# Optimization experiments

Measured on AMD Instinct MI355X. Metric: run time of the kernel, lower is better.

The kernel has to match this reference:

```python
import jax, jax.numpy as jnp
import numpy as np
import math

B, H, L, D = 4, 16, 8192, 64


def setup_inputs() -> dict:
    key = jax.random.key(0)
    kq, kk, kv, kmu = jax.random.split(key, 4)
    Q = jax.random.normal(kq, (B, H, L, D), dtype=jnp.float32)
    K = jax.random.normal(kk, (B, H, L, D), dtype=jnp.float32)
    V = jax.random.normal(kv, (B, H, L, D), dtype=jnp.float32)
    mask = jnp.ones((B, L), dtype=jnp.float32)
    # learned params (multi_gauss=True): pi init [0.5,0.5]; mu ~ N(0,0.5) with mu[0]=0
    pi = jnp.array([0.5, 0.5], dtype=jnp.float32)
    mu = jax.random.normal(kmu, (2, H, D), dtype=jnp.float32) * 0.5
    mu = mu * jnp.array([0.0, 1.0], dtype=jnp.float32)[:, None, None]
    return {"Q": Q, "K": K, "V": V, "mask": mask, "pi": pi, "mu": mu}


def reference(Q, K, V, mask, pi, mu):
    # mixture-of-Gaussian keys: shift K by two learned means, convex-combine
    p = jnp.clip(pi, 0.0, 1.0)
    K1 = K - mu[0][None, :, None, :]
    K2 = K - mu[1][None, :, None, :]
    Km = K1 * p[0] + K2 * p[1]
    # kernelized linear attention: phi(x) = elu(x)+1, scaled by 1/L^0.25
    L_ = Q.shape[2]
    s = 1.0 / math.sqrt(math.sqrt(L_))
    m = mask[:, None, :, None]  # [B,1,L,1]
    Qf = (jax.nn.elu(Q) + 1.0) * s
    Kf = (jax.nn.elu(Km) + 1.0) * m * s
    Vm = V * m
    # K^T V first: [B,H,D,D] state, then Q @ state -> [B,H,L,D]
    KV = jnp.einsum('bhld,bhle->bhde', Kf, Vm)
    return jnp.einsum('bhld,bhde->bhle', Qf, KV)
```

## Files before the change

kernel.cpp:

```cpp
#include <hip/hip_runtime.h>
#include <cstddef>

#define B_ 4
#define H_ 16
#define L_ 8192
#define D_ 64
#define BH_ (B_ * H_)

#define SCALE 0.1051120519067143f

__device__ __forceinline__ float elu1(float x) {
    return x > 0.0f ? (x + 1.0f) : __expf(x);
}

__global__ __launch_bounds__(256) void zero_kernel(float4* __restrict__ p) {
    p[(size_t)blockIdx.x * 256 + threadIdx.x] = make_float4(0.f, 0.f, 0.f, 0.f);
}

__global__ __launch_bounds__(256) void kv_kernel(
    const float* __restrict__ K, const float* __restrict__ V,
    const float* __restrict__ mask, const float* __restrict__ pi,
    const float* __restrict__ mu, float* __restrict__ kv)
{
    const int bh = blockIdx.x;
    const int b = bh >> 4;
    const int h = bh & 15;
    const int l0 = blockIdx.y * 512;
    const int t = threadIdx.x;
    const int lane_e = t & 63;
    const int dbase = (t >> 6) * 16;

    __shared__ float muc[64];
    __shared__ float sK[32][64];
    __shared__ float sV[32][64];

    float p0 = fminf(fmaxf(pi[0], 0.f), 1.f);
    float p1 = fminf(fmaxf(pi[1], 0.f), 1.f);
    const float psum = p0 + p1;
    if (t < 64) {
        muc[t] = p0 * mu[h * D_ + t] + p1 * mu[(H_ + h) * D_ + t];
    }
    __syncthreads();

    const float* Kb = K + (size_t)bh * L_ * D_;
    const float* Vb = V + (size_t)bh * L_ * D_;
    const float* mb = mask + (size_t)b * L_;

    const int r0 = t >> 4;
    const int c0 = (t & 15) * 4;
    const int r1 = (t + 256) >> 4;
    const int c1 = c0;

    const float4 mu0 = *(const float4*)&muc[c0];
    const float4 mu1 = *(const float4*)&muc[c1];

    float acc[16];
#pragma unroll
    for (int i = 0; i < 16; ++i) acc[i] = 0.f;

    for (int tile = 0; tile < 512; tile += 32) {
        const int lb = l0 + tile;
        {
            const int l = lb + r0;
            const float m = mb[l];
            const float sm = SCALE * m;
            float4 k = *(const float4*)(Kb + (size_t)l * D_ + c0);
            float4 o;
            o.x = elu1(k.x * psum - mu0.x) * sm;
            o.y = elu1(k.y * psum - mu0.y) * sm;
            o.z = elu1(k.z * psum - mu0.z) * sm;
            o.w = elu1(k.w * psum - mu0.w) * sm;
            *(float4*)&sK[r0][c0] = o;
            float4 v = *(const float4*)(Vb + (size_t)l * D_ + c0);
            v.x *= m; v.y *= m; v.z *= m; v.w *= m;
            *(float4*)&sV[r0][c0] = v;
        }
        {
            const int l = lb + r1;
            const float m = mb[l];
            const float sm = SCALE * m;
            float4 k = *(const float4*)(Kb + (size_t)l * D_ + c1);
            float4 o;
            o.x = elu1(k.x * psum - mu1.x) * sm;
            o.y = elu1(k.y * psum - mu1.y) * sm;
            o.z = elu1(k.z * psum - mu1.z) * sm;
            o.w = elu1(k.w * psum - mu1.w) * sm;
            *(float4*)&sK[r1][c1] = o;
            float4 v = *(const float4*)(Vb + (size_t)l * D_ + c1);
            v.x *= m; v.y *= m; v.z *= m; v.w *= m;
            *(float4*)&sV[r1][c1] = v;
        }
        __syncthreads();

#pragma unroll
        for (int l = 0; l < 32; ++l) {
            const float v = sV[l][lane_e];
            const float4 ka = *(const float4*)&sK[l][dbase];
            const float4 kb = *(const float4*)&sK[l][dbase + 4];
            const float4 kc = *(const float4*)&sK[l][dbase + 8];
            const float4 kd = *(const float4*)&sK[l][dbase + 12];
            acc[0]  += ka.x * v;  acc[1]  += ka.y * v;
            acc[2]  += ka.z * v;  acc[3]  += ka.w * v;
            acc[4]  += kb.x * v;  acc[5]  += kb.y * v;
            acc[6]  += kb.z * v;  acc[7]  += kb.w * v;
            acc[8]  += kc.x * v;  acc[9]  += kc.y * v;
            acc[10] += kc.z * v;  acc[11] += kc.w * v;
            acc[12] += kd.x * v;  acc[13] += kd.y * v;
            acc[14] += kd.z * v;  acc[15] += kd.w * v;
        }
        __syncthreads();
    }

    float* kvp = kv + (size_t)bh * (D_ * D_);
#pragma unroll
    for (int j = 0; j < 16; ++j)
        atomicAdd(kvp + (dbase + j) * D_ + lane_e, acc[j]);
}

__global__ __launch_bounds__(256) void out_kernel(
    const float* __restrict__ Q, const float* __restrict__ kv,
    float* __restrict__ out)
{
    const int bh = blockIdx.x;
    const int l0 = blockIdx.y * 64;
    const int t = threadIdx.x;

    __shared__ float sKV[64][64];
    __shared__ float sQ[64][65];

    const float* Qb = Q + (size_t)bh * L_ * D_ + (size_t)l0 * D_;
    const float* kvp = kv + (size_t)bh * (D_ * D_);

#pragma unroll
    for (int i = 0; i < 4; ++i) {
        const int idx = t + i * 256;
        *(float4*)&sKV[idx >> 4][(idx & 15) * 4] = *(const float4*)(kvp + (size_t)idx * 4);
    }
#pragma unroll
    for (int i = 0; i < 4; ++i) {
        const int idx = t + i * 256;
        const int row = idx >> 4;
        const int col = (idx & 15) * 4;
        const float4 q = *(const float4*)(Qb + (size_t)idx * 4);
        sQ[row][col + 0] = elu1(q.x) * SCALE;
        sQ[row][col + 1] = elu1(q.y) * SCALE;
        sQ[row][col + 2] = elu1(q.z) * SCALE;
        sQ[row][col + 3] = elu1(q.w) * SCALE;
    }
    __syncthreads();

    const int te = t & 15;
    const int tl = t >> 4;
    const int e0 = te * 4;
    const int lb = tl * 4;

    float acc[16];
#pragma unroll
    for (int i = 0; i < 16; ++i) acc[i] = 0.f;

#pragma unroll 16
    for (int d = 0; d < 64; ++d) {
        const float4 k4 = *(const float4*)&sKV[d][e0];
        const float q0 = sQ[lb + 0][d];
        const float q1 = sQ[lb + 1][d];
        const float q2 = sQ[lb + 2][d];
        const float q3 = sQ[lb + 3][d];
        acc[0]  += q0 * k4.x;  acc[1]  += q0 * k4.y;
        acc[2]  += q0 * k4.z;  acc[3]  += q0 * k4.w;
        acc[4]  += q1 * k4.x;  acc[5]  += q1 * k4.y;
        acc[6]  += q1 * k4.z;  acc[7]  += q1 * k4.w;
        acc[8]  += q2 * k4.x;  acc[9]  += q2 * k4.y;
        acc[10] += q2 * k4.z;  acc[11] += q2 * k4.w;
        acc[12] += q3 * k4.x;  acc[13] += q3 * k4.y;
        acc[14] += q3 * k4.z;  acc[15] += q3 * k4.w;
    }

    float* ob = out + (size_t)bh * L_ * D_ + (size_t)l0 * D_;
#pragma unroll
    for (int i = 0; i < 4; ++i) {
        float4 r;
        r.x = acc[i * 4 + 0];
        r.y = acc[i * 4 + 1];
        r.z = acc[i * 4 + 2];
        r.w = acc[i * 4 + 3];
        *(float4*)(ob + (size_t)(lb + i) * D_ + e0) = r;
    }
}

extern "C" void kernel_launch(void* const* d_in, const int* in_sizes, int n_in,
                              void* d_out, int out_size, void* d_ws, size_t ws_size,
                              hipStream_t stream) {
    (void)in_sizes; (void)n_in; (void)out_size; (void)ws_size;
    const float* Q    = (const float*)d_in[0];
    const float* K    = (const float*)d_in[1];
    const float* V    = (const float*)d_in[2];
    const float* mask = (const float*)d_in[3];
    const float* pi   = (const float*)d_in[4];
    const float* mu   = (const float*)d_in[5];
    float* out = (float*)d_out;
    float* kvw = (float*)d_ws;

    zero_kernel<<<256, 256, 0, stream>>>((float4*)kvw);
    kv_kernel<<<dim3(BH_, 16), 256, 0, stream>>>(K, V, mask, pi, mu, kvw);
    out_kernel<<<dim3(BH_, 128), 256, 0, stream>>>(Q, kvw, out);
}
```

Baseline: 436.7 us.

## Use 8x8 register tiles in both kernels and bf16 LDS staging for output

The KV-state kernel now gives each thread an 8x8 register tile of the DxD outer product. V is read straight from global memory and only transformed K is staged in LDS. Per-wave partial states are reduced in shared memory before one atomic pass per block. The output kernel handles 256 rows per block with an 8x8 tile per thread, storing Q (transposed) and the KV state as bf16 in LDS to halve LDS traffic. The goal is fewer LDS reads per FMA and less atomic contention, at the cost of bf16 rounding error in the output and high register pressure from 64 accumulators.

```diff
diff --git a/kernel.cpp b/kernel.cpp
--- a/kernel.cpp
+++ b/kernel.cpp
@@ -1,189 +1,209 @@
 #include <hip/hip_runtime.h>
 #include <cstddef>
+#include <stdint.h>
 
 #define B_ 4
 #define H_ 16
 #define L_ 8192
 #define D_ 64
-#define BH_ (B_ * H_)
+#define BH_ 64
 
 #define SCALE 0.1051120519067143f
 
 __device__ __forceinline__ float elu1(float x) {
     return x > 0.0f ? (x + 1.0f) : __expf(x);
 }
+__device__ __forceinline__ unsigned short f2bf_rne(float x) {
+    unsigned u = __float_as_uint(x);
+    u += 0x7fffu + ((u >> 16) & 1u);
+    return (unsigned short)(u >> 16);
+}
+__device__ __forceinline__ float bf_lo(unsigned w) { return __uint_as_float(w << 16); }
+__device__ __forceinline__ float bf_hi(unsigned w) { return __uint_as_float(w & 0xffff0000u); }
 
 __global__ __launch_bounds__(256) void zero_kernel(float4* __restrict__ p) {
     p[(size_t)blockIdx.x * 256 + threadIdx.x] = make_float4(0.f, 0.f, 0.f, 0.f);
 }
 
-__global__ __launch_bounds__(256) void kv_kernel(
+#define CH1 16
+#define ROWS1 (L_ / CH1)
+#define TR1 64
+#define SKLD 68
+
+__global__ __launch_bounds__(256, 4) void kv_kernel(
     const float* __restrict__ K, const float* __restrict__ V,
     const float* __restrict__ mask, const float* __restrict__ pi,
     const float* __restrict__ mu, float* __restrict__ kv)
 {
+    __shared__ float sK[TR1 * SKLD];
+    __shared__ float muc[64];
+
     const int bh = blockIdx.x;
-    const int b = bh >> 4;
-    const int h = bh & 15;
-    const int l0 = blockIdx.y * 512;
-    const int t = threadIdx.x;
-    const int lane_e = t & 63;
-    const int dbase = (t >> 6) * 16;
-
-    __shared__ float muc[64];
-    __shared__ float sK[32][64];
-    __shared__ float sV[32][64];
-
-    float p0 = fminf(fmaxf(pi[0], 0.f), 1.f);
-    float p1 = fminf(fmaxf(pi[1], 0.f), 1.f);
+    const int b  = bh >> 4;
+    const int h  = bh & 15;
+    const int l0 = blockIdx.y * ROWS1;
+    const int t  = threadIdx.x;
+    const int wave = t >> 6;
+    const int lane = t & 63;
+    const int d0 = (lane >> 3) * 8;
+    const int e0 = (lane & 7) * 8;
+
+    const float p0 = fminf(fmaxf(pi[0], 0.f), 1.f);
+    const float p1 = fminf(fmaxf(pi[1], 0.f), 1.f);
     const float psum = p0 + p1;
-    if (t < 64) {
-        muc[t] = p0 * mu[h * D_ + t] + p1 * mu[(H_ + h) * D_ + t];
-    }
+    if (t < 64) muc[t] = p0 * mu[h * 64 + t] + p1 * mu[1024 + h * 64 + t];
+
+    const float* Kb = K + (size_t)bh * (L_ * 64);
+    const float* Vb = V + (size_t)bh * (L_ * 64);
+    const float* mb = mask + (size_t)b * L_;
+
+    const int trow = t >> 2;
+    const int tc   = (t & 3) * 16;
+
+    float acc[64];
+#pragma unroll
+    for (int i = 0; i < 64; ++i) acc[i] = 0.f;
+
+#pragma unroll 1
+    for (int tile = 0; tile < ROWS1; tile += TR1) {
+        const int base = l0 + tile;
+        __syncthreads();
+        {
+            const int row = base + trow;
+            const float m = mb[row];
+            const float sm2 = SCALE * m * m;
+            const float* kp = Kb + (size_t)row * 64 + tc;
+#pragma unroll
+            for (int q = 0; q < 4; ++q) {
+                float4 kk = *(const float4*)(kp + 4 * q);
+                float4 mm = *(const float4*)(&muc[tc + 4 * q]);
+                float4 o;
+                o.x = elu1(kk.x * psum - mm.x) * sm2;
+                o.y = elu1(kk.y * psum - mm.y) * sm2;
+                o.z = elu1(kk.z * psum - mm.z) * sm2;
+                o.w = elu1(kk.w * psum - mm.w) * sm2;
+                *(float4*)&sK[trow * SKLD + tc + 4 * q] = o;
+            }
+        }
+        __syncthreads();
+#pragma unroll
+        for (int j = 0; j < 16; ++j) {
+            const int r = wave + 4 * j;
+            const float* vp = Vb + (size_t)(base + r) * 64 + e0;
+            const float4 va = *(const float4*)(vp);
+            const float4 vb = *(const float4*)(vp + 4);
+            const float4 ka = *(const float4*)&sK[r * SKLD + d0];
+            const float4 kb = *(const float4*)&sK[r * SKLD + d0 + 4];
+            const float kf[8] = {ka.x, ka.y, ka.z, ka.w, kb.x, kb.y, kb.z, kb.w};
+            const float vf[8] = {va.x, va.y, va.z, va.w, vb.x, vb.y, vb.z, vb.w};
+#pragma unroll
+            for (int i = 0; i < 8; ++i)
+#pragma unroll
+                for (int jj = 0; jj < 8; ++jj)
+                    acc[i * 8 + jj] = fmaf(kf[i], vf[jj], acc[i * 8 + jj]);
+        }
+    }
+
     __syncthreads();
-
-    const float* Kb = K + (size_t)bh * L_ * D_;
-    const float* Vb = V + (size_t)bh * L_ * D_;
-    const float* mb = mask + (size_t)b * L_;
-
-    const int r0 = t >> 4;
-    const int c0 = (t & 15) * 4;
-    const int r1 = (t + 256) >> 4;
-    const int c1 = c0;
-
-    const float4 mu0 = *(const float4*)&muc[c0];
-    const float4 mu1 = *(const float4*)&muc[c1];
-
-    float acc[16];
-#pragma unroll
-    for (int i = 0; i < 16; ++i) acc[i] = 0.f;
-
-    for (int tile = 0; tile < 512; tile += 32) {
-        const int lb = l0 + tile;
-        {
-            const int l = lb + r0;
-            const float m = mb[l];
-            const float sm = SCALE * m;
-            float4 k = *(const float4*)(Kb + (size_t)l * D_ + c0);
-            float4 o;
-            o.x = elu1(k.x * psum - mu0.x) * sm;
-            o.y = elu1(k.y * psum - mu0.y) * sm;
-            o.z = elu1(k.z * psum - mu0.z) * sm;
-            o.w = elu1(k.w * psum - mu0.w) * sm;
-            *(float4*)&sK[r0][c0] = o;
-            float4 v = *(const float4*)(Vb + (size_t)l * D_ + c0);
-            v.x *= m; v.y *= m; v.z *= m; v.w *= m;
-            *(float4*)&sV[r0][c0] = v;
-        }
-        {
-            const int l = lb + r1;
-            const float m = mb[l];
-            const float sm = SCALE * m;
-            float4 k = *(const float4*)(Kb + (size_t)l * D_ + c1);
-            float4 o;
-            o.x = elu1(k.x * psum - mu1.x) * sm;
-            o.y = elu1(k.y * psum - mu1.y) * sm;
-            o.z = elu1(k.z * psum - mu1.z) * sm;
-            o.w = elu1(k.w * psum - mu1.w) * sm;
-            *(float4*)&sK[r1][c1] = o;
-            float4 v = *(const float4*)(Vb + (size_t)l * D_ + c1);
-            v.x *= m; v.y *= m; v.z *= m; v.w *= m;
-            *(float4*)&sV[r1][c1] = v;
+    float* red = sK;
+#pragma unroll 1
+    for (int w = 0; w < 4; ++w) {
+        if (wave == w) {
+#pragma unroll
+            for (int i = 0; i < 8; ++i)
+#pragma unroll
+                for (int jj = 0; jj < 8; ++jj) {
+                    const int idx = (d0 + i) * 64 + e0 + jj;
+                    red[idx] = (w == 0) ? acc[i * 8 + jj] : red[idx] + acc[i * 8 + jj];
+                }
         }
         __syncthreads();
-
-#pragma unroll
-        for (int l = 0; l < 32; ++l) {
-            const float v = sV[l][lane_e];
-            const float4 ka = *(const float4*)&sK[l][dbase];
-            const float4 kb = *(const float4*)&sK[l][dbase + 4];
-            const float4 kc = *(const float4*)&sK[l][dbase + 8];
-            const float4 kd = *(const float4*)&sK[l][dbase + 12];
-            acc[0]  += ka.x * v;  acc[1]  += ka.y * v;
-            acc[2]  += ka.z * v;  acc[3]  += ka.w * v;
-            acc[4]  += kb.x * v;  acc[5]  += kb.y * v;
-            acc[6]  += kb.z * v;  acc[7]  += kb.w * v;
-            acc[8]  += kc.x * v;  acc[9]  += kc.y * v;
-            acc[10] += kc.z * v;  acc[11] += kc.w * v;
-            acc[12] += kd.x * v;  acc[13] += kd.y * v;
-            acc[14] += kd.z * v;  acc[15] += kd.w * v;
-        }
-        __syncthreads();
-    }
-
-    float* kvp = kv + (size_t)bh * (D_ * D_);
-#pragma unroll
-    for (int j = 0; j < 16; ++j)
-        atomicAdd(kvp + (dbase + j) * D_ + lane_e, acc[j]);
-}
-
-__global__ __launch_bounds__(256) void out_kernel(
+    }
+
+    float* kvb = kv + (size_t)bh * 4096;
+#pragma unroll
+    for (int k = 0; k < 16; ++k)
+        atomicAdd(kvb + k * 256 + t, red[k * 256 + t]);
+}
+
+#define ROWS2 256
+
+__global__ __launch_bounds__(256, 3) void out_kernel(
     const float* __restrict__ Q, const float* __restrict__ kv,
     float* __restrict__ out)
 {
+    __shared__ unsigned short skv[64 * 64];
+    __shared__ unsigned short sqt[4][64 * 64];
+
     const int bh = blockIdx.x;
-    const int l0 = blockIdx.y * 64;
+    const int l0 = blockIdx.y * ROWS2;
     const int t = threadIdx.x;
-
-    __shared__ float sKV[64][64];
-    __shared__ float sQ[64][65];
-
-    const float* Qb = Q + (size_t)bh * L_ * D_ + (size_t)l0 * D_;
-    const float* kvp = kv + (size_t)bh * (D_ * D_);
-
-#pragma unroll
-    for (int i = 0; i < 4; ++i) {
-        const int idx = t + i * 256;
-        *(float4*)&sKV[idx >> 4][(idx & 15) * 4] = *(const float4*)(kvp + (size_t)idx * 4);
-    }
-#pragma unroll
-    for (int i = 0; i < 4; ++i) {
-        const int idx = t + i * 256;
-        const int row = idx >> 4;
-        const int col = (idx & 15) * 4;
-        const float4 q = *(const float4*)(Qb + (size_t)idx * 4);
-        sQ[row][col + 0] = elu1(q.x) * SCALE;
-        sQ[row][col + 1] = elu1(q.y) * SCALE;
-        sQ[row][col + 2] = elu1(q.z) * SCALE;
-        sQ[row][col + 3] = elu1(q.w) * SCALE;
+    const int wave = t >> 6;
+    const int lane = t & 63;
+    const int r0 = (lane >> 3) * 8;
+    const int e0 = (lane & 7) * 8;
+
+    {
+        const float* kvb = kv + (size_t)bh * 4096 + t * 16;
+        unsigned w[8];
+#pragma unroll
+        for (int q = 0; q < 4; ++q) {
+            float4 f = *(const float4*)(kvb + 4 * q);
+            w[2 * q + 0] = (unsigned)f2bf_rne(f.x) | ((unsigned)f2bf_rne(f.y) << 16);
+            w[2 * q + 1] = (unsigned)f2bf_rne(f.z) | ((unsigned)f2bf_rne(f.w) << 16);
+        }
+        *(uint4*)&skv[t * 16 + 0] = make_uint4(w[0], w[1], w[2], w[3]);
+        *(uint4*)&skv[t * 16 + 8] = make_uint4(w[4], w[5], w[6], w[7]);
+    }
+    {
+        const int row = l0 + wave * 64 + lane;
+        const float* qp = Q + (size_t)bh * (L_ * 64) + (size_t)row * 64;
+        unsigned short* qt = &sqt[wave][0];
+#pragma unroll
+        for (int c4 = 0; c4 < 16; ++c4) {
+            float4 q = *(const float4*)(qp + 4 * c4);
+            qt[(4 * c4 + 0) * 64 + lane] = f2bf_rne(elu1(q.x) * SCALE);
+            qt[(4 * c4 + 1) * 64 + lane] = f2bf_rne(elu1(q.y) * SCALE);
+            qt[(4 * c4 + 2) * 64 + lane] = f2bf_rne(elu1(q.z) * SCALE);
+            qt[(4 * c4 + 3) * 64 + lane] = f2bf_rne(elu1(q.w) * SCALE);
+        }
     }
     __syncthreads();
 
-    const int te = t & 15;
-    const int tl = t >> 4;
-    const int e0 = te * 4;
-    const int lb = tl * 4;
-
-    float acc[16];
-#pragma unroll
-    for (int i = 0; i < 16; ++i) acc[i] = 0.f;
-
-#pragma unroll 16
-    for (int d = 0; d < 64; ++d) {
-        const float4 k4 = *(const float4*)&sKV[d][e0];
-        const float q0 = sQ[lb + 0][d];
-        const float q1 = sQ[lb + 1][d];
-        const float q2 = sQ[lb + 2][d];
-        const float q3 = sQ[lb + 3][d];
-        acc[0]  += q0 * k4.x;  acc[1]  += q0 * k4.y;
-        acc[2]  += q0 * k4.z;  acc[3]  += q0 * k4.w;
-        acc[4]  += q1 * k4.x;  acc[5]  += q1 * k4.y;
-        acc[6]  += q1 * k4.z;  acc[7]  += q1 * k4.w;
-        acc[8]  += q2 * k4.x;  acc[9]  += q2 * k4.y;
-        acc[10] += q2 * k4.z;  acc[11] += q2 * k4.w;
-        acc[12] += q3 * k4.x;  acc[13] += q3 * k4.y;
-        acc[14] += q3 * k4.z;  acc[15] += q3 * k4.w;
-    }
-
-    float* ob = out + (size_t)bh * L_ * D_ + (size_t)l0 * D_;
-#pragma unroll
-    for (int i = 0; i < 4; ++i) {
-        float4 r;
-        r.x = acc[i * 4 + 0];
-        r.y = acc[i * 4 + 1];
-        r.z = acc[i * 4 + 2];
-        r.w = acc[i * 4 + 3];
-        *(float4*)(ob + (size_t)(lb + i) * D_ + e0) = r;
+    float acc[64];
+#pragma unroll
+    for (int i = 0; i < 64; ++i) acc[i] = 0.f;
+
+    const unsigned short* qt = &sqt[wave][0];
+#pragma unroll 1
+    for (int c = 0; c < 16; ++c) {
+#pragma unroll
+        for (int k = 0; k < 4; ++k) {
+            const int d = 4 * c + k;
+            const uint4 qw = *(const uint4*)&qt[d * 64 + r0];
+            const uint4 kw = *(const uint4*)&skv[d * 64 + e0];
+            const float qf[8] = {bf_lo(qw.x), bf_hi(qw.x), bf_lo(qw.y), bf_hi(qw.y),
+                                 bf_lo(qw.z), bf_hi(qw.z), bf_lo(qw.w), bf_hi(qw.w)};
+            const float kf[8] = {bf_lo(kw.x), bf_hi(kw.x), bf_lo(kw.y), bf_hi(kw.y),
+                                 bf_lo(kw.z), bf_hi(kw.z), bf_lo(kw.w), bf_hi(kw.w)};
+#pragma unroll
+            for (int i = 0; i < 8; ++i)
+#pragma unroll
+                for (int j = 0; j < 8; ++j)
+                    acc[i * 8 + j] = fmaf(qf[i], kf[j], acc[i * 8 + j]);
+        }
+    }
+
+    float* ob = out + (size_t)bh * (L_ * 64) + (size_t)(l0 + wave * 64 + r0) * 64 + e0;
+#pragma unroll
+    for (int i = 0; i < 8; ++i) {
+        float4 oa, obv;
+        oa.x = acc[i * 8 + 0]; oa.y = acc[i * 8 + 1];
+        oa.z = acc[i * 8 + 2]; oa.w = acc[i * 8 + 3];
+        obv.x = acc[i * 8 + 4]; obv.y = acc[i * 8 + 5];
+        obv.z = acc[i * 8 + 6]; obv.w = acc[i * 8 + 7];
+        *(float4*)(ob + (size_t)i * 64) = oa;
+        *(float4*)(ob + (size_t)i * 64 + 4) = obv;
     }
 }
 
@@ -201,6 +221,6 @@
     float* kvw = (float*)d_ws;
 
     zero_kernel<<<256, 256, 0, stream>>>((float4*)kvw);
-    kv_kernel<<<dim3(BH_, 16), 256, 0, stream>>>(K, V, mask, pi, mu, kvw);
-    out_kernel<<<dim3(BH_, 128), 256, 0, stream>>>(Q, kvw, out);
-}
+    kv_kernel<<<dim3(BH_, CH1), 256, 0, stream>>>(K, V, mask, pi, mu, kvw);
+    out_kernel<<<dim3(BH_, L_ / ROWS2), 256, 0, stream>>>(Q, kvw, out);
+}
```

After: 518.8 us. 1.19x slower.
